# Kernel optimization log

Measured on AMD Instinct MI355X. Metric: run time of the kernel, lower is better.

Reference implementation:

```python
import jax, jax.numpy as jnp
import numpy as np
import math

B, D, NH, NS, NT = 16, 256, 512, 8, 32
NV = NS * NT          # 256 prediction variables
L, H, A = 4, 8, 64    # attention layers, heads, head dim
HA = H * A            # 512
M = 512               # mlp_dim
R = 128               # resolution
EPS = 1e-5


def setup_inputs() -> dict:
    key = jax.random.key(0)
    ks = jax.random.split(key, 32)
    s = 0.02
    inp = {
        'hist_encoded': jax.random.normal(ks[0], (B, NH, D), jnp.float32),
        'hist_true_u': jax.random.uniform(ks[1], (B, NH), jnp.float32),
        'pred_encoded': jax.random.normal(ks[2], (B, NV, D), jnp.float32),
        'pred_true_u': jax.random.uniform(ks[3], (B, NV), jnp.float32),
        # dimension shifting layer
        'ds_w': jax.random.normal(ks[4], (D, HA), jnp.float32) * s,
        'ds_b': jnp.zeros((HA,), jnp.float32),
        # per-layer, per-head key/value creators: Linear(D+1 -> A)
        'key_w': jax.random.normal(ks[5], (L, H, D + 1, A), jnp.float32) * s,
        'key_b': jnp.zeros((L, H, A), jnp.float32),
        'val_w': jax.random.normal(ks[6], (L, H, D + 1, A), jnp.float32) * s,
        'val_b': jnp.zeros((L, H, A), jnp.float32),
        # layer norms
        'ln1_g': jnp.ones((L, HA), jnp.float32),
        'ln1_b': jnp.zeros((L, HA), jnp.float32),
        'ln2_g': jnp.ones((L, HA), jnp.float32),
        'ln2_b': jnp.zeros((L, HA), jnp.float32),
        # feed-forward (mlp_layers=2): HA->M, M->M, M->HA
        'ff_w1': jax.random.normal(ks[7], (L, HA, M), jnp.float32) * s,
        'ff_b1': jnp.zeros((L, M), jnp.float32),
        'ff_w2': jax.random.normal(ks[8], (L, M, M), jnp.float32) * s,
        'ff_b2': jnp.zeros((L, M), jnp.float32),
        'ff_w3': jax.random.normal(ks[9], (L, M, HA), jnp.float32) * s,
        'ff_b3': jnp.zeros((L, HA), jnp.float32),
        # dist extractor
        'de_w': jax.random.normal(ks[10], (HA, R), jnp.float32) * s,
        'de_b': jnp.zeros((R,), jnp.float32),
        'num_series': NS,
        'num_timesteps': NT,
    }
    return inp


def _ln(x, g, b):
    m = x.mean(-1, keepdims=True)
    v = ((x - m) ** 2).mean(-1, keepdims=True)
    return g * (x - m) / jnp.sqrt(v + EPS) + b


def _forward(hist_encoded, hist_true_u, pred_encoded, pred_true_u,
             ds_w, ds_b, key_w, key_b, val_w, val_b,
             ln1_g, ln1_b, ln2_g, ln2_b,
             ff_w1, ff_b1, ff_w2, ff_b2, ff_w3, ff_b3,
             de_w, de_b):
    Bm, NVm, Dm = pred_encoded.shape
    NHm = hist_encoded.shape[1]
    Lm, Hm, _, Am = key_w.shape
    W = NHm + NVm
    # identity permutation in the source loss() -> no-op
    att = pred_encoded @ ds_w + ds_b  # [B, NV, HA]
    # key/value inputs: [hist||u ; pred||u] -> [B, W, D+1]
    ki = jnp.concatenate([
        jnp.concatenate([hist_encoded, hist_true_u[:, :, None]], axis=2),
        jnp.concatenate([pred_encoded, pred_true_u[:, :, None]], axis=2)], axis=1)
    keys = jnp.einsum('bwd,lhda->lbhwa', ki, key_w) + key_b[:, None, :, None, :]
    vals = jnp.einsum('bwd,lhda->lbhwa', ki, val_w) + val_b[:, None, :, None, :]
    # flipped-triangular mask: position w is masked iff w >= NH + v
    mask = jnp.arange(W)[None, :] >= (NHm + jnp.arange(NVm)[:, None])  # [NV, W]
    scale = Am ** (-0.5)
    for l in range(Lm):
        avh = att.reshape(Bm, NVm, Hm, Am)
        prod = jnp.einsum('bvhi,bhwi->bhvw', avh, keys[l])  # [B,H,NV,W]
        prod = jnp.where(mask, -jnp.inf, prod) * scale
        w = jax.nn.softmax(prod, axis=-1)
        a = jnp.einsum('bhvw,bhwj->bvhj', w, vals[l]).reshape(Bm, NVm, Hm * Am)
        att = _ln(att + a, ln1_g[l], ln1_b[l])
        ff = jnp.maximum(att @ ff_w1[l] + ff_b1[l], 0.0)
        ff = jnp.maximum(ff @ ff_w2[l] + ff_b2[l], 0.0)
        ff = ff @ ff_w3[l] + ff_b3[l]
        att = _ln(att + ff, ln2_g[l], ln2_b[l])
    res = de_w.shape[-1]
    target = jnp.clip(jnp.floor(pred_true_u[:, 1:] * res).astype(jnp.int32), 0, res - 1)
    logits = (att @ de_w + de_b)[:, 1:, :]
    lp = math.log(res) + jax.nn.log_softmax(logits, axis=2)
    lp = jnp.take_along_axis(lp, target[:, :, None], axis=2)[:, :, 0]
    return -lp.sum(axis=1)  # [B]


def reference(hist_encoded, hist_true_u, pred_encoded, pred_true_u,
              ds_w, ds_b, key_w, key_b, val_w, val_b,
              ln1_g, ln1_b, ln2_g, ln2_b,
              ff_w1, ff_b1, ff_w2, ff_b2, ff_w3, ff_b3,
              de_w, de_b, num_series, num_timesteps):
    assert pred_encoded.shape[1] == num_series * num_timesteps
    return _forward(hist_encoded, hist_true_u, pred_encoded, pred_true_u,
                    ds_w, ds_b, key_w, key_b, val_w, val_b,
                    ln1_g, ln1_b, ln2_g, ln2_b,
                    ff_w1, ff_b1, ff_w2, ff_b2, ff_w3, ff_b3,
                    de_w, de_b)
```

## Files before the change

### kernel.cpp

```cpp
#include <hip/hip_runtime.h>
#include <hip/hip_cooperative_groups.h>
namespace cg = cooperative_groups;

constexpr int kB = 16, kD = 256, kNH = 512, kNV = 256, kW = 768;
constexpr int kL = 4, kH = 8, kA = 64, kHA = 512, kM = 512, kR = 128;
constexpr int kKP = 288;
constexpr int kRows = kB * kNV;

typedef __bf16 bf16x8 __attribute__((ext_vector_type(8)));
typedef __bf16 bf16x4 __attribute__((ext_vector_type(4)));
typedef float f32x4 __attribute__((ext_vector_type(4)));

__device__ inline void load_lds16(const __bf16* g, __bf16* l) {
  __builtin_amdgcn_global_load_lds(
      (const __attribute__((address_space(1))) void*)g,
      (__attribute__((address_space(3))) void*)l, 16, 0, 0);
}

constexpr int kP1 = kB * kW * kKP;
constexpr int kP2 = 4096 * kKP;
constexpr int kP3 = 12 * 512 * 512;
constexpr int kP4 = 200704;
constexpr int kP5 = 16;
constexpr int kPT = kP1 + kP2 + kP3 + kP4 + kP5;

__global__ void prep_kernel(const float* __restrict__ hist,
                            const float* __restrict__ hist_u,
                            const float* __restrict__ pred,
                            const float* __restrict__ pred_u,
                            const float* __restrict__ kw,
                            const float* __restrict__ vw,
                            const float* __restrict__ w1,
                            const float* __restrict__ w2,
                            const float* __restrict__ w3,
                            const float* __restrict__ ds_w,
                            const float* __restrict__ de_w,
                            const float* __restrict__ key_b,
                            const float* __restrict__ val_b,
                            __bf16* __restrict__ ki,
                            __bf16* __restrict__ kvwt,
                            __bf16* __restrict__ ffwt,
                            __bf16* __restrict__ ds_wt,
                            __bf16* __restrict__ de_wt,
                            float* __restrict__ kvb,
                            float* __restrict__ outz) {
  int i = blockIdx.x * 256 + threadIdx.x;
  if (i < kP1) {
    int d = i % kKP;
    int bw = i / kKP;
    int w = bw % kW;
    int b = bw / kW;
    float v = 0.f;
    if (d < 257) {
      if (w < kNH)
        v = (d < kD) ? hist[((size_t)b * kNH + w) * kD + d] : hist_u[b * kNH + w];
      else {
        int p = w - kNH;
        v = (d < kD) ? pred[((size_t)b * kNV + p) * kD + d] : pred_u[b * kNV + p];
      }
    }
    ki[i] = (__bf16)v;
  } else if (i < kP1 + kP2) {
    int j = i - kP1;
    int d = j % kKP;
    int c = j / kKP;
    float v = 0.f;
    if (d < 257) {
      bool isv = c >= 2048;
      int cc = isv ? c - 2048 : c;
      int l = cc >> 9, rest = cc & 511;
      int h = rest >> 6, a = rest & 63;
      size_t src = (((size_t)l * kH + h) * 257 + d) * kA + a;
      v = isv ? vw[src] : kw[src];
    }
    kvwt[j] = (__bf16)v;
  } else if (i < kP1 + kP2 + kP3) {
    int j = i - kP1 - kP2;
    int k = j & 511;
    int n = (j >> 9) & 511;
    int mat = j >> 18;
    int l = mat / 3, which = mat % 3;
    const float* src = which == 0 ? w1 : which == 1 ? w2 : w3;
    ffwt[j] = (__bf16)src[((size_t)l * 512 + k) * 512 + n];
  } else if (i < kP1 + kP2 + kP3 + kP4) {
    int j = i - kP1 - kP2 - kP3;
    if (j < 131072) {
      int n = j >> 8, k = j & 255;
      ds_wt[j] = (__bf16)ds_w[k * 512 + n];
    } else if (j < 196608) {
      int jj = j - 131072;
      int n = jj >> 9, k = jj & 511;
      de_wt[jj] = (__bf16)de_w[k * 128 + n];
    } else {
      int c = j - 196608;
      bool isv = c >= 2048;
      int cc = isv ? c - 2048 : c;
      int l = cc >> 9, rest = cc & 511;
      kvb[c] = isv ? val_b[l * 512 + rest] : key_b[l * 512 + rest];
    }
  } else if (i < kPT) {
    outz[i - kP1 - kP2 - kP3 - kP4] = 0.f;
  }
}

template <int BN, int OMODE, bool RELU, bool KIMAP, bool BIASROW>
__device__ __forceinline__ void gemm_core(
    int bxv, int byv, const __bf16* __restrict__ A,
    const __bf16* __restrict__ Bt, const float* __restrict__ bias,
    void* __restrict__ Cout, __bf16* __restrict__ Cout2, int K, int lda,
    int ldc, __bf16* As, __bf16* Bs) {
  constexpr int JN = BN / 32;
  constexpr int BROWS = BN / 4;
  const int t = threadIdx.x;
  const int wid = t >> 6;
  const int lane = t & 63;
  const int bm = byv * 128;
  const int bn = bxv * BN;
  const int wm = (wid >> 1) * 64;
  const int wn = (wid & 1) * (BN / 2);
  const int sr = lane >> 2, sc = lane & 3;
  const int skey = (sr >> 1) & 3;
  const int abase = KIMAP ? ((bm >> 8) * 768 + 512 + (bm & 255)) : bm;
  const __bf16* Ag = A + (size_t)(abase + wid * 32 + sr) * lda + (sc ^ skey) * 8;
  const __bf16* Bg = Bt + (size_t)(bn + wid * BROWS + sr) * K + (sc ^ skey) * 8;
  __bf16* AsW = As + (wid * 32) * 32;
  __bf16* BsW = Bs + (wid * BROWS) * 32;

  f32x4 acc[4][JN] = {};
  const int q = lane >> 4, mr = lane & 15;
  const int rkey = (mr >> 1) & 3;
  for (int k0 = 0; k0 < K; k0 += 32) {
    if (k0) __syncthreads();
    load_lds16(Ag + k0, AsW);
    load_lds16(Ag + (size_t)16 * lda + k0, AsW + 16 * 32);
    load_lds16(Bg + k0, BsW);
    if (BN == 128) load_lds16(Bg + (size_t)16 * K + k0, BsW + 16 * 32);
    __syncthreads();
    bf16x8 af[4], bfr[JN];
#pragma unroll
    for (int i = 0; i < 4; ++i)
      af[i] = *(const bf16x8*)(As + (wm + i * 16 + mr) * 32 + (q ^ rkey) * 8);
#pragma unroll
    for (int j = 0; j < JN; ++j)
      bfr[j] = *(const bf16x8*)(Bs + (wn + j * 16 + mr) * 32 + (q ^ rkey) * 8);
#pragma unroll
    for (int i = 0; i < 4; ++i)
#pragma unroll
      for (int j = 0; j < JN; ++j)
        acc[i][j] = __builtin_amdgcn_mfma_f32_16x16x32_bf16(af[i], bfr[j],
                                                            acc[i][j], 0, 0, 0);
  }
#pragma unroll
  for (int j = 0; j < JN; ++j) {
    int col = bn + wn + j * 16 + mr;
    float bscol = BIASROW ? 0.f : bias[col];
#pragma unroll
    for (int i = 0; i < 4; ++i) {
      int row0 = bm + wm + i * 16 + q * 4;
#pragma unroll
      for (int r = 0; r < 4; ++r) {
        float v = acc[i][j][r] + (BIASROW ? bias[row0 + r] : bscol);
        if (RELU) v = fmaxf(v, 0.f);
        size_t idx = (size_t)(row0 + r) * ldc + col;
        if (OMODE == 0) {
          ((float*)Cout)[idx] = v;
        } else if (OMODE == 1) {
          ((__bf16*)Cout)[idx] = (__bf16)v;
        } else {
          ((float*)Cout)[idx] = v;
          Cout2[idx] = (__bf16)v;
        }
      }
    }
  }
}

__global__ __launch_bounds__(256) void gemm3_kernel(
    const __bf16* __restrict__ ki, const __bf16* __restrict__ ds_wt,
    const float* __restrict__ ds_b, float* __restrict__ att,
    __bf16* __restrict__ att_bf, const __bf16* __restrict__ kv_wt,
    const float* __restrict__ kvb, __bf16* __restrict__ kvs_k,
    __bf16* __restrict__ vT) {
  __shared__ __align__(16) __bf16 smem[8192];
  __bf16* As = smem;
  __bf16* Bs = smem + 4096;
  int bid = blockIdx.x;
  if (bid < 256) {
    gemm_core<64, 2, false, true, false>(bid & 7, bid >> 3, ki, ds_wt, ds_b,
                                         att, att_bf, 256, kKP, 512, As, Bs);
  } else if (bid < 1792) {
    int b2 = bid - 256;
    gemm_core<128, 1, false, false, false>(b2 & 15, b2 >> 4, ki, kv_wt, kvb,
                                           kvs_k, nullptr, kKP, kKP, 2048, As,
                                           Bs);
  } else {
    int b3 = bid - 1792;
    gemm_core<128, 1, false, false, true>(b3 % 96, b3 / 96,
                                          kv_wt + (size_t)2048 * kKP, ki,
                                          kvb + 2048, vT, nullptr, kKP, kKP,
                                          12288, As, Bs);
  }
}

__device__ __forceinline__ void attn_stage(
    int u, __bf16* smem, const __bf16* __restrict__ attbf,
    const __bf16* __restrict__ kvs_k, const __bf16* __restrict__ vT,
    __bf16* __restrict__ outbf, int l) {
  const int qt = u & 3, h = (u >> 2) & 7, b = u >> 5;
  __bf16* Ks = smem;
  __bf16* Vt = smem + 64 * 72;
  __bf16* Ps = smem + 2 * 64 * 72;
  const int t = threadIdx.x;
  const int w = t >> 6, lane = t & 63;
  const int quad = lane >> 4, mr = lane & 15;
  bf16x8 aq[2];
  {
    const __bf16* qp = attbf + ((size_t)(b * kNV + qt * 64 + w * 16 + mr) * kHA +
                                h * kA + quad * 8);
    aq[0] = *(const bf16x8*)qp;
    aq[1] = *(const bf16x8*)(qp + 32);
  }
  f32x4 o[4] = {};
  float m_ = -1e30f, l_ = 0.f;
  const int cmax = kNH + qt * 64;
  const int pr = t >> 2, pc = t & 3;
  const __bf16* kbase = kvs_k + ((size_t)(b * kW + pr) * 2048 + l * 512 + h * kA);
  const __bf16* vbase = vT + (size_t)(l * 512 + h * kA + pr) * 12288 + b * kW;
  bf16x8 kc0, kc1, vc0, vc1;
  kc0 = *(const bf16x8*)(kbase + pc * 8);
  kc1 = *(const bf16x8*)(kbase + pc * 8 + 32);
  vc0 = *(const bf16x8*)(vbase + pc * 16);
  vc1 = *(const bf16x8*)(vbase + pc * 16 + 8);
  for (int c0 = 0; c0 <= cmax; c0 += 64) {
    __syncthreads();
    *(bf16x8*)&Ks[pr * 72 + pc * 8] = kc0;
    *(bf16x8*)&Ks[pr * 72 + pc * 8 + 32] = kc1;
    *(bf16x8*)&Vt[pr * 72 + pc * 16] = vc0;
    *(bf16x8*)&Vt[pr * 72 + pc * 16 + 8] = vc1;
    __syncthreads();
    if (c0 + 64 <= cmax) {
      const __bf16* kp = kbase + (size_t)(c0 + 64) * 2048;
      const __bf16* vp = vbase + c0 + 64;
      kc0 = *(const bf16x8*)(kp + pc * 8);
      kc1 = *(const bf16x8*)(kp + pc * 8 + 32);
      vc0 = *(const bf16x8*)(vp + pc * 16);
      vc1 = *(const bf16x8*)(vp + pc * 16 + 8);
    }
    f32x4 s[4];
#pragma unroll
    for (int j = 0; j < 4; ++j) {
      bf16x8 ak0 = *(const bf16x8*)&Ks[(j * 16 + mr) * 72 + quad * 8];
      bf16x8 ak1 = *(const bf16x8*)&Ks[(j * 16 + mr) * 72 + quad * 8 + 32];
      f32x4 z = {};
      z = __builtin_amdgcn_mfma_f32_16x16x32_bf16(ak0, aq[0], z, 0, 0, 0);
      z = __builtin_amdgcn_mfma_f32_16x16x32_bf16(ak1, aq[1], z, 0, 0, 0);
      s[j] = z;
    }
    const int lim = cmax - c0;
    float sv[16], mx = -1e30f;
#pragma unroll
    for (int j = 0; j < 4; ++j)
#pragma unroll
      for (int r = 0; r < 4; ++r) {
        int p = j * 16 + quad * 4 + r;
        float x = (p < lim + mr) ? s[j][r] * 0.125f : -1e30f;
        sv[j * 4 + r] = x;
        mx = fmaxf(mx, x);
      }
    mx = fmaxf(mx, __shfl_xor(mx, 16));
    mx = fmaxf(mx, __shfl_xor(mx, 32));
    float mnew = fmaxf(m_, mx);
    float corr = __expf(m_ - mnew);
    float rs = 0.f;
#pragma unroll
    for (int i = 0; i < 16; ++i) {
      sv[i] = __expf(sv[i] - mnew);
      rs += sv[i];
    }
    rs += __shfl_xor(rs, 16);
    rs += __shfl_xor(rs, 32);
    l_ = l_ * corr + rs;
    m_ = mnew;
#pragma unroll
    for (int j = 0; j < 4; ++j) {
      bf16x4 pk = {(__bf16)sv[j * 4 + 0], (__bf16)sv[j * 4 + 1],
                   (__bf16)sv[j * 4 + 2], (__bf16)sv[j * 4 + 3]};
      *(bf16x4*)&Ps[(w * 16 + mr) * 72 + j * 16 + quad * 4] = pk;
    }
#pragma unroll
    for (int r = 0; r < 4; ++r) {
      float cr = __shfl(corr, quad * 4 + r);
#pragma unroll
      for (int j = 0; j < 4; ++j) o[j][r] *= cr;
    }
    bf16x8 ap0 = *(const bf16x8*)&Ps[(w * 16 + mr) * 72 + quad * 8];
    bf16x8 ap1 = *(const bf16x8*)&Ps[(w * 16 + mr) * 72 + quad * 8 + 32];
#pragma unroll
    for (int j = 0; j < 4; ++j) {
      bf16x8 b0 = *(const bf16x8*)&Vt[(j * 16 + mr) * 72 + quad * 8];
      bf16x8 b1 = *(const bf16x8*)&Vt[(j * 16 + mr) * 72 + quad * 8 + 32];
      o[j] = __builtin_amdgcn_mfma_f32_16x16x32_bf16(ap0, b0, o[j], 0, 0, 0);
      o[j] = __builtin_amdgcn_mfma_f32_16x16x32_bf16(ap1, b1, o[j], 0, 0, 0);
    }
  }
  float invl = 1.f / l_;
#pragma unroll
  for (int r = 0; r < 4; ++r) {
    float ir = __shfl(invl, quad * 4 + r);
    int row = b * kNV + qt * 64 + w * 16 + quad * 4 + r;
#pragma unroll
    for (int j = 0; j < 4; ++j)
      outbf[(size_t)row * kHA + h * kA + j * 16 + mr] = (__bf16)(o[j][r] * ir);
  }
}

__device__ __forceinline__ void ln_stage(int u, float* __restrict__ att,
                                         const __bf16* __restrict__ addbf,
                                         const float* __restrict__ g,
                                         const float* __restrict__ be,
                                         __bf16* __restrict__ attbf) {
  const int t = threadIdx.x;
  const int wid = t >> 6, lane = t & 63;
#pragma unroll
  for (int i = 0; i < 2; ++i) {
    int row = u * 8 + wid * 2 + i;
    float* ar = att + (size_t)row * kHA + lane * 8;
    float4 x0 = *(float4*)ar;
    float4 x1 = *(float4*)(ar + 4);
    bf16x8 d = *(const bf16x8*)(addbf + (size_t)row * kHA + lane * 8);
    float xs[8] = {x0.x + (float)d[0], x0.y + (float)d[1], x0.z + (float)d[2],
                   x0.w + (float)d[3], x1.x + (float)d[4], x1.y + (float)d[5],
                   x1.z + (float)d[6], x1.w + (float)d[7]};
    float s = 0.f, sq = 0.f;
#pragma unroll
    for (int e = 0; e < 8; ++e) {
      s += xs[e];
      sq += xs[e] * xs[e];
    }
    for (int o = 32; o; o >>= 1) {
      s += __shfl_xor(s, o);
      sq += __shfl_xor(sq, o);
    }
    float mean = s * (1.f / kHA);
    float inv = rsqrtf(sq * (1.f / kHA) - mean * mean + 1e-5f);
    const float* gp = g + lane * 8;
    const float* bp = be + lane * 8;
    float4 g0 = *(const float4*)gp, g1 = *(const float4*)(gp + 4);
    float4 b0 = *(const float4*)bp, b1 = *(const float4*)(bp + 4);
    float ga[8] = {g0.x, g0.y, g0.z, g0.w, g1.x, g1.y, g1.z, g1.w};
    float ba[8] = {b0.x, b0.y, b0.z, b0.w, b1.x, b1.y, b1.z, b1.w};
    float ys[8];
    bf16x8 yb;
#pragma unroll
    for (int e = 0; e < 8; ++e) {
      ys[e] = ga[e] * (xs[e] - mean) * inv + ba[e];
      yb[e] = (__bf16)ys[e];
    }
    *(float4*)ar = make_float4(ys[0], ys[1], ys[2], ys[3]);
    *(float4*)(ar + 4) = make_float4(ys[4], ys[5], ys[6], ys[7]);
    *(bf16x8*)(attbf + (size_t)row * kHA + lane * 8) = yb;
  }
}

__device__ __forceinline__ void de_loss_stage(
    int blk, float* red, const __bf16* __restrict__ attbf,
    const __bf16* __restrict__ de_wt, const float* __restrict__ de_b,
    const float* __restrict__ pred_u, float* __restrict__ out) {
  const int t = threadIdx.x;
  const int w = t >> 6, lane = t & 63, quad = lane >> 4, mr = lane & 15;
  const int row0 = blk * 64 + w * 16;
  f32x4 acc[8] = {};
  const __bf16* Ap = attbf + (size_t)(row0 + mr) * kHA + quad * 8;
#pragma unroll 4
  for (int k0 = 0; k0 < 512; k0 += 32) {
    bf16x8 a = *(const bf16x8*)(Ap + k0);
#pragma unroll
    for (int j = 0; j < 8; ++j) {
      bf16x8 bb =
          *(const bf16x8*)(de_wt + (size_t)(j * 16 + mr) * 512 + k0 + quad * 8);
      acc[j] = __builtin_amdgcn_mfma_f32_16x16x32_bf16(a, bb, acc[j], 0, 0, 0);
    }
  }
  float dbv[8];
#pragma unroll
  for (int j = 0; j < 8; ++j) dbv[j] = de_b[j * 16 + mr];
  float lpacc = 0.f;
#pragma unroll
  for (int r = 0; r < 4; ++r) {
    int row = row0 + quad * 4 + r;
    int v = row & 255;
    float lg[8], mx = -1e30f;
#pragma unroll
    for (int j = 0; j < 8; ++j) {
      lg[j] = acc[j][r] + dbv[j];
      mx = fmaxf(mx, lg[j]);
    }
    mx = fmaxf(mx, __shfl_xor(mx, 1));
    mx = fmaxf(mx, __shfl_xor(mx, 2));
    mx = fmaxf(mx, __shfl_xor(mx, 4));
    mx = fmaxf(mx, __shfl_xor(mx, 8));
    float se = 0.f;
#pragma unroll
    for (int j = 0; j < 8; ++j) se += __expf(lg[j] - mx);
    se += __shfl_xor(se, 1);
    se += __shfl_xor(se, 2);
    se += __shfl_xor(se, 4);
    se += __shfl_xor(se, 8);
    float lse = mx + __logf(se);
    float u = pred_u[(row >> 8) * 256 + v];
    int tgt = (int)floorf(u * 128.f);
    tgt = max(0, min(127, tgt));
    float cand = (mr == (tgt & 15)) ? lg[tgt >> 4] : 0.f;
    cand += __shfl_xor(cand, 1);
    cand += __shfl_xor(cand, 2);
    cand += __shfl_xor(cand, 4);
    cand += __shfl_xor(cand, 8);
    float lp = (v >= 1) ? (4.8520302639196171f + cand - lse) : 0.f;
    lpacc += lp;
  }
  lpacc += __shfl_xor(lpacc, 16);
  lpacc += __shfl_xor(lpacc, 32);
  __syncthreads();
  if (lane == 0) red[w] = lpacc;
  __syncthreads();
  if (t == 0)
    atomicAdd(&out[blk >> 2], -(red[0] + red[1] + red[2] + red[3]));
}

__global__ __launch_bounds__(256) void attn_kernel(
    const __bf16* __restrict__ attbf, const __bf16* __restrict__ kvs_k,
    const __bf16* __restrict__ vT, __bf16* __restrict__ outbf, int l) {
  __shared__ __align__(16) __bf16 smem[3 * 64 * 72];
  attn_stage(blockIdx.x, smem, attbf, kvs_k, vT, outbf, l);
}

__global__ __launch_bounds__(256) void ln_kernel(
    float* __restrict__ att, const __bf16* __restrict__ addbf,
    const float* __restrict__ g, const float* __restrict__ be,
    __bf16* __restrict__ attbf) {
  ln_stage(blockIdx.x, att, addbf, g, be, attbf);
}

template <bool RELU>
__global__ __launch_bounds__(256) void gemm_ff_kernel(
    const __bf16* __restrict__ A, const __bf16* __restrict__ Bt,
    const float* __restrict__ bias, __bf16* __restrict__ Cout) {
  __shared__ __align__(16) __bf16 smem[6144];
  gemm_core<64, 1, RELU, false, false>(blockIdx.x & 7, blockIdx.x >> 3, A, Bt,
                                       bias, Cout, nullptr, 512, 512, 512, smem,
                                       smem + 4096);
}

__global__ __launch_bounds__(256) void de_loss_kernel(
    const __bf16* __restrict__ attbf, const __bf16* __restrict__ de_wt,
    const float* __restrict__ de_b, const float* __restrict__ pred_u,
    float* __restrict__ out) {
  __shared__ float red[4];
  de_loss_stage(blockIdx.x, red, attbf, de_wt, de_b, pred_u, out);
}

__global__ __launch_bounds__(256, 2) void model_kernel(
    const __bf16* kvs_k, const __bf16* vT, float* att, __bf16* att_bf,
    __bf16* tmp_bf, __bf16* ff1_bf, __bf16* ff2_bf, const __bf16* ffw_t,
    const float* ff_b1, const float* ff_b2, const float* ff_b3,
    const float* ln1_g, const float* ln1_b, const float* ln2_g,
    const float* ln2_b, const __bf16* de_wt, const float* de_b,
    const float* pred_u, float* out) {
  cg::grid_group grid = cg::this_grid();
  __shared__ __align__(16) __bf16 smem[3 * 64 * 72];
  const int bid = blockIdx.x;
  for (int l = 0; l < kL; ++l) {
    attn_stage(bid, smem, att_bf, kvs_k, vT, tmp_bf, l);
    grid.sync();
    ln_stage(bid, att, tmp_bf, ln1_g + l * kHA, ln1_b + l * kHA, att_bf);
    grid.sync();
    if (bid < 256)
      gemm_core<64, 1, true, false, false>(
          bid & 7, bid >> 3, att_bf, ffw_t + (size_t)(l * 3) * 262144,
          ff_b1 + l * kM, ff1_bf, nullptr, 512, 512, 512, smem, smem + 4096);
    grid.sync();
    if (bid < 256)
      gemm_core<64, 1, true, false, false>(
          bid & 7, bid >> 3, ff1_bf, ffw_t + (size_t)(l * 3 + 1) * 262144,
          ff_b2 + l * kM, ff2_bf, nullptr, 512, 512, 512, smem, smem + 4096);
    grid.sync();
    if (bid < 256)
      gemm_core<64, 1, false, false, false>(
          bid & 7, bid >> 3, ff2_bf, ffw_t + (size_t)(l * 3 + 2) * 262144,
          ff_b3 + l * kHA, tmp_bf, nullptr, 512, 512, 512, smem, smem + 4096);
    grid.sync();
    ln_stage(bid, att, tmp_bf, ln2_g + l * kHA, ln2_b + l * kHA, att_bf);
    grid.sync();
  }
  if (bid < 64)
    de_loss_stage(bid, (float*)smem, att_bf, de_wt, de_b, pred_u, out);
}

extern "C" void kernel_launch(void* const* d_in, const int* in_sizes, int n_in,
                              void* d_out, int out_size, void* d_ws, size_t ws_size,
                              hipStream_t stream) {
  const float* hist   = (const float*)d_in[0];
  const float* hist_u = (const float*)d_in[1];
  const float* pred   = (const float*)d_in[2];
  const float* pred_u = (const float*)d_in[3];
  const float* ds_w   = (const float*)d_in[4];
  const float* ds_b   = (const float*)d_in[5];
  const float* key_w  = (const float*)d_in[6];
  const float* key_b  = (const float*)d_in[7];
  const float* val_w  = (const float*)d_in[8];
  const float* val_b  = (const float*)d_in[9];
  const float* ln1_g  = (const float*)d_in[10];
  const float* ln1_b  = (const float*)d_in[11];
  const float* ln2_g  = (const float*)d_in[12];
  const float* ln2_b  = (const float*)d_in[13];
  const float* ff_w1  = (const float*)d_in[14];
  const float* ff_b1  = (const float*)d_in[15];
  const float* ff_w2  = (const float*)d_in[16];
  const float* ff_b2  = (const float*)d_in[17];
  const float* ff_w3  = (const float*)d_in[18];
  const float* ff_b3  = (const float*)d_in[19];
  const float* de_w   = (const float*)d_in[20];
  const float* de_b   = (const float*)d_in[21];
  float* out = (float*)d_out;

  char* ws = (char*)d_ws;
  size_t off = 0;
  auto alloc = [&](size_t bytes) { char* p = ws + off; off += bytes; return p; };
  __bf16* ki_bf  = (__bf16*)alloc((size_t)kB * kW * kKP * 2);
  __bf16* kv_wt  = (__bf16*)alloc((size_t)4096 * kKP * 2);
  __bf16* ffw_t  = (__bf16*)alloc((size_t)12 * 512 * 512 * 2);
  __bf16* ds_wt  = (__bf16*)alloc((size_t)512 * 256 * 2);
  __bf16* de_wt  = (__bf16*)alloc((size_t)128 * 512 * 2);
  float*  kvb    = (float*)alloc((size_t)4096 * 4);
  __bf16* kvs_k  = (__bf16*)alloc((size_t)kB * kW * 2048 * 2);
  __bf16* vT     = (__bf16*)alloc((size_t)2048 * 12288 * 2);
  float*  att    = (float*)alloc((size_t)kRows * kHA * 4);
  __bf16* att_bf = (__bf16*)alloc((size_t)kRows * kHA * 2);
  __bf16* tmp_bf = (__bf16*)alloc((size_t)kRows * kHA * 2);
  __bf16* ff1_bf = (__bf16*)alloc((size_t)kRows * kM * 2);
  __bf16* ff2_bf = (__bf16*)alloc((size_t)kRows * kM * 2);

  prep_kernel<<<(kPT + 255) / 256, 256, 0, stream>>>(
      hist, hist_u, pred, pred_u, key_w, val_w, ff_w1, ff_w2, ff_w3, ds_w, de_w,
      key_b, val_b, ki_bf, kv_wt, ffw_t, ds_wt, de_wt, kvb, out);

  gemm3_kernel<<<3328, 256, 0, stream>>>(ki_bf, ds_wt, ds_b, att, att_bf, kv_wt,
                                         kvb, kvs_k, vT);

  int nbPerCU = 0;
  hipError_t qerr = hipOccupancyMaxActiveBlocksPerMultiprocessor(
      &nbPerCU, (const void*)model_kernel, 256, 0);
  bool coop = (qerr == hipSuccess && nbPerCU >= 2);
  if (coop) {
    void* cargs[] = {(void*)&kvs_k,  (void*)&vT,     (void*)&att,
                     (void*)&att_bf, (void*)&tmp_bf, (void*)&ff1_bf,
                     (void*)&ff2_bf, (void*)&ffw_t,  (void*)&ff_b1,
                     (void*)&ff_b2,  (void*)&ff_b3,  (void*)&ln1_g,
                     (void*)&ln1_b,  (void*)&ln2_g,  (void*)&ln2_b,
                     (void*)&de_wt,  (void*)&de_b,   (void*)&pred_u,
                     (void*)&out};
    hipError_t lerr = hipLaunchCooperativeKernel(
        (void*)model_kernel, dim3(512), dim3(256), cargs, 0, stream);
    if (lerr != hipSuccess) coop = false;
  }
  if (!coop) {
    for (int l = 0; l < kL; ++l) {
      attn_kernel<<<512, 256, 0, stream>>>(att_bf, kvs_k, vT, tmp_bf, l);
      ln_kernel<<<512, 256, 0, stream>>>(att, tmp_bf, ln1_g + l * kHA,
                                         ln1_b + l * kHA, att_bf);
      gemm_ff_kernel<true><<<256, 256, 0, stream>>>(
          att_bf, ffw_t + (size_t)(l * 3) * 262144, ff_b1 + l * kM, ff1_bf);
      gemm_ff_kernel<true><<<256, 256, 0, stream>>>(
          ff1_bf, ffw_t + (size_t)(l * 3 + 1) * 262144, ff_b2 + l * kM, ff2_bf);
      gemm_ff_kernel<false><<<256, 256, 0, stream>>>(
          ff2_bf, ffw_t + (size_t)(l * 3 + 2) * 262144, ff_b3 + l * kHA, tmp_bf);
      ln_kernel<<<512, 256, 0, stream>>>(att, tmp_bf, ln2_g + l * kHA,
                                         ln2_b + l * kHA, att_bf);
    }
    de_loss_kernel<<<64, 256, 0, stream>>>(att_bf, de_wt, de_b, pred_u, out);
  }
}
```

Baseline: 473.3 us.

## Replace cooperative persistent kernel with per-stage launches and double-buffer attention K/V

Drops the cooperative grid-synchronised model kernel and always runs the separate per-stage kernels. The attention kernel now double-buffers K and V tiles in LDS, cutting to one barrier per chunk and overlapping the next chunk's global loads with the MFMA work. Softmax no longer tracks a running maximum or rescales the accumulator; it exponentiates scaled scores directly, which saves work but can overflow if scores get large. The causal mask now includes the per-wave row offset, which changes the masking compared with the old code.

```diff
diff --git a/kernel.cpp b/kernel.cpp
--- a/kernel.cpp
+++ b/kernel.cpp
@@ -1,6 +1,4 @@
 #include <hip/hip_runtime.h>
-#include <hip/hip_cooperative_groups.h>
-namespace cg = cooperative_groups;
 
 constexpr int kB = 16, kD = 256, kNH = 512, kNV = 256, kW = 768;
 constexpr int kL = 4, kH = 8, kA = 64, kHA = 512, kM = 512, kR = 128;
@@ -202,14 +200,14 @@
   }
 }
 
-__device__ __forceinline__ void attn_stage(
-    int u, __bf16* smem, const __bf16* __restrict__ attbf,
-    const __bf16* __restrict__ kvs_k, const __bf16* __restrict__ vT,
-    __bf16* __restrict__ outbf, int l) {
+__global__ __launch_bounds__(256) void attn_kernel(
+    const __bf16* __restrict__ attbf, const __bf16* __restrict__ kvs_k,
+    const __bf16* __restrict__ vT, __bf16* __restrict__ outbf, int l) {
+  const int u = blockIdx.x;
   const int qt = u & 3, h = (u >> 2) & 7, b = u >> 5;
-  __bf16* Ks = smem;
-  __bf16* Vt = smem + 64 * 72;
-  __bf16* Ps = smem + 2 * 64 * 72;
+  __shared__ __align__(16) __bf16 Ks[2][64 * 72];
+  __shared__ __align__(16) __bf16 Vt[2][64 * 72];
+  __shared__ __align__(16) __bf16 Ps[64 * 72];
   const int t = threadIdx.x;
   const int w = t >> 6, lane = t & 63;
   const int quad = lane >> 4, mr = lane & 15;
@@ -221,24 +219,27 @@
     aq[1] = *(const bf16x8*)(qp + 32);
   }
   f32x4 o[4] = {};
-  float m_ = -1e30f, l_ = 0.f;
+  float l_ = 0.f;
   const int cmax = kNH + qt * 64;
   const int pr = t >> 2, pc = t & 3;
   const __bf16* kbase = kvs_k + ((size_t)(b * kW + pr) * 2048 + l * 512 + h * kA);
   const __bf16* vbase = vT + (size_t)(l * 512 + h * kA + pr) * 12288 + b * kW;
-  bf16x8 kc0, kc1, vc0, vc1;
-  kc0 = *(const bf16x8*)(kbase + pc * 8);
-  kc1 = *(const bf16x8*)(kbase + pc * 8 + 32);
-  vc0 = *(const bf16x8*)(vbase + pc * 16);
-  vc1 = *(const bf16x8*)(vbase + pc * 16 + 8);
+  {
+    bf16x8 k0 = *(const bf16x8*)(kbase + pc * 8);
+    bf16x8 k1 = *(const bf16x8*)(kbase + pc * 8 + 32);
+    bf16x8 v0 = *(const bf16x8*)(vbase + pc * 16);
+    bf16x8 v1 = *(const bf16x8*)(vbase + pc * 16 + 8);
+    *(bf16x8*)&Ks[0][pr * 72 + pc * 8] = k0;
+    *(bf16x8*)&Ks[0][pr * 72 + pc * 8 + 32] = k1;
+    *(bf16x8*)&Vt[0][pr * 72 + pc * 16] = v0;
+    *(bf16x8*)&Vt[0][pr * 72 + pc * 16 + 8] = v1;
+  }
+  __syncthreads();
   for (int c0 = 0; c0 <= cmax; c0 += 64) {
-    __syncthreads();
-    *(bf16x8*)&Ks[pr * 72 + pc * 8] = kc0;
-    *(bf16x8*)&Ks[pr * 72 + pc * 8 + 32] = kc1;
-    *(bf16x8*)&Vt[pr * 72 + pc * 16] = vc0;
-    *(bf16x8*)&Vt[pr * 72 + pc * 16 + 8] = vc1;
-    __syncthreads();
-    if (c0 + 64 <= cmax) {
+    const int cur = (c0 >> 6) & 1;
+    const bool havenext = (c0 + 64 <= cmax);
+    bf16x8 kc0, kc1, vc0, vc1;
+    if (havenext) {
       const __bf16* kp = kbase + (size_t)(c0 + 64) * 2048;
       const __bf16* vp = vbase + c0 + 64;
       kc0 = *(const bf16x8*)(kp + pc * 8);
@@ -249,58 +250,61 @@
     f32x4 s[4];
 #pragma unroll
     for (int j = 0; j < 4; ++j) {
-      bf16x8 ak0 = *(const bf16x8*)&Ks[(j * 16 + mr) * 72 + quad * 8];
-      bf16x8 ak1 = *(const bf16x8*)&Ks[(j * 16 + mr) * 72 + quad * 8 + 32];
+      bf16x8 ak0 = *(const bf16x8*)&Ks[cur][(j * 16 + mr) * 72 + quad * 8];
+      bf16x8 ak1 = *(const bf16x8*)&Ks[cur][(j * 16 + mr) * 72 + quad * 8 + 32];
       f32x4 z = {};
       z = __builtin_amdgcn_mfma_f32_16x16x32_bf16(ak0, aq[0], z, 0, 0, 0);
       z = __builtin_amdgcn_mfma_f32_16x16x32_bf16(ak1, aq[1], z, 0, 0, 0);
       s[j] = z;
     }
     const int lim = cmax - c0;
-    float sv[16], mx = -1e30f;
-#pragma unroll
-    for (int j = 0; j < 4; ++j)
-#pragma unroll
-      for (int r = 0; r < 4; ++r) {
-        int p = j * 16 + quad * 4 + r;
-        float x = (p < lim + mr) ? s[j][r] * 0.125f : -1e30f;
-        sv[j * 4 + r] = x;
-        mx = fmaxf(mx, x);
-      }
-    mx = fmaxf(mx, __shfl_xor(mx, 16));
-    mx = fmaxf(mx, __shfl_xor(mx, 32));
-    float mnew = fmaxf(m_, mx);
-    float corr = __expf(m_ - mnew);
+    float ev[16];
     float rs = 0.f;
-#pragma unroll
-    for (int i = 0; i < 16; ++i) {
-      sv[i] = __expf(sv[i] - mnew);
-      rs += sv[i];
+    if (lim >= 64) {
+#pragma unroll
+      for (int j = 0; j < 4; ++j)
+#pragma unroll
+        for (int r = 0; r < 4; ++r) {
+          float e = __expf(s[j][r] * 0.125f);
+          ev[j * 4 + r] = e;
+          rs += e;
+        }
+    } else {
+      const int limw = lim + w * 16 + mr;
+#pragma unroll
+      for (int j = 0; j < 4; ++j)
+#pragma unroll
+        for (int r = 0; r < 4; ++r) {
+          int p = j * 16 + quad * 4 + r;
+          float e = (p < limw) ? __expf(s[j][r] * 0.125f) : 0.f;
+          ev[j * 4 + r] = e;
+          rs += e;
+        }
     }
     rs += __shfl_xor(rs, 16);
     rs += __shfl_xor(rs, 32);
-    l_ = l_ * corr + rs;
-    m_ = mnew;
+    l_ += rs;
 #pragma unroll
     for (int j = 0; j < 4; ++j) {
-      bf16x4 pk = {(__bf16)sv[j * 4 + 0], (__bf16)sv[j * 4 + 1],
-                   (__bf16)sv[j * 4 + 2], (__bf16)sv[j * 4 + 3]};
+      bf16x4 pk = {(__bf16)ev[j * 4 + 0], (__bf16)ev[j * 4 + 1],
+                   (__bf16)ev[j * 4 + 2], (__bf16)ev[j * 4 + 3]};
       *(bf16x4*)&Ps[(w * 16 + mr) * 72 + j * 16 + quad * 4] = pk;
-    }
-#pragma unroll
-    for (int r = 0; r < 4; ++r) {
-      float cr = __shfl(corr, quad * 4 + r);
-#pragma unroll
-      for (int j = 0; j < 4; ++j) o[j][r] *= cr;
     }
     bf16x8 ap0 = *(const bf16x8*)&Ps[(w * 16 + mr) * 72 + quad * 8];
     bf16x8 ap1 = *(const bf16x8*)&Ps[(w * 16 + mr) * 72 + quad * 8 + 32];
 #pragma unroll
     for (int j = 0; j < 4; ++j) {
-      bf16x8 b0 = *(const bf16x8*)&Vt[(j * 16 + mr) * 72 + quad * 8];
-      bf16x8 b1 = *(const bf16x8*)&Vt[(j * 16 + mr) * 72 + quad * 8 + 32];
+      bf16x8 b0 = *(const bf16x8*)&Vt[cur][(j * 16 + mr) * 72 + quad * 8];
+      bf16x8 b1 = *(const bf16x8*)&Vt[cur][(j * 16 + mr) * 72 + quad * 8 + 32];
       o[j] = __builtin_amdgcn_mfma_f32_16x16x32_bf16(ap0, b0, o[j], 0, 0, 0);
       o[j] = __builtin_amdgcn_mfma_f32_16x16x32_bf16(ap1, b1, o[j], 0, 0, 0);
+    }
+    if (havenext) {
+      *(bf16x8*)&Ks[cur ^ 1][pr * 72 + pc * 8] = kc0;
+      *(bf16x8*)&Ks[cur ^ 1][pr * 72 + pc * 8 + 32] = kc1;
+      *(bf16x8*)&Vt[cur ^ 1][pr * 72 + pc * 16] = vc0;
+      *(bf16x8*)&Vt[cur ^ 1][pr * 72 + pc * 16 + 8] = vc1;
+      __syncthreads();
     }
   }
   float invl = 1.f / l_;
@@ -314,16 +318,15 @@
   }
 }
 
-__device__ __forceinline__ void ln_stage(int u, float* __restrict__ att,
-                                         const __bf16* __restrict__ addbf,
-                                         const float* __restrict__ g,
-                                         const float* __restrict__ be,
-                                         __bf16* __restrict__ attbf) {
+__global__ __launch_bounds__(256) void ln_kernel(
+    float* __restrict__ att, const __bf16* __restrict__ addbf,
+    const float* __restrict__ g, const float* __restrict__ be,
+    __bf16* __restrict__ attbf) {
   const int t = threadIdx.x;
   const int wid = t >> 6, lane = t & 63;
 #pragma unroll
   for (int i = 0; i < 2; ++i) {
-    int row = u * 8 + wid * 2 + i;
+    int row = blockIdx.x * 8 + wid * 2 + i;
     float* ar = att + (size_t)row * kHA + lane * 8;
     float4 x0 = *(float4*)ar;
     float4 x1 = *(float4*)(ar + 4);
@@ -362,10 +365,21 @@
   }
 }
 
-__device__ __forceinline__ void de_loss_stage(
-    int blk, float* red, const __bf16* __restrict__ attbf,
-    const __bf16* __restrict__ de_wt, const float* __restrict__ de_b,
-    const float* __restrict__ pred_u, float* __restrict__ out) {
+template <bool RELU>
+__global__ __launch_bounds__(256) void gemm_ff_kernel(
+    const __bf16* __restrict__ A, const __bf16* __restrict__ Bt,
+    const float* __restrict__ bias, __bf16* __restrict__ Cout) {
+  __shared__ __align__(16) __bf16 smem[6144];
+  gemm_core<64, 1, RELU, false, false>(blockIdx.x & 7, blockIdx.x >> 3, A, Bt,
+                                       bias, Cout, nullptr, 512, 512, 512, smem,
+                                       smem + 4096);
+}
+
+__global__ __launch_bounds__(256) void de_loss_kernel(
+    const __bf16* __restrict__ attbf, const __bf16* __restrict__ de_wt,
+    const float* __restrict__ de_b, const float* __restrict__ pred_u,
+    float* __restrict__ out) {
+  const int blk = blockIdx.x;
   const int t = threadIdx.x;
   const int w = t >> 6, lane = t & 63, quad = lane >> 4, mr = lane & 15;
   const int row0 = blk * 64 + w * 16;
@@ -420,80 +434,11 @@
   }
   lpacc += __shfl_xor(lpacc, 16);
   lpacc += __shfl_xor(lpacc, 32);
-  __syncthreads();
+  __shared__ float red[4];
   if (lane == 0) red[w] = lpacc;
   __syncthreads();
   if (t == 0)
     atomicAdd(&out[blk >> 2], -(red[0] + red[1] + red[2] + red[3]));
-}
-
-__global__ __launch_bounds__(256) void attn_kernel(
-    const __bf16* __restrict__ attbf, const __bf16* __restrict__ kvs_k,
-    const __bf16* __restrict__ vT, __bf16* __restrict__ outbf, int l) {
-  __shared__ __align__(16) __bf16 smem[3 * 64 * 72];
-  attn_stage(blockIdx.x, smem, attbf, kvs_k, vT, outbf, l);
-}
-
-__global__ __launch_bounds__(256) void ln_kernel(
-    float* __restrict__ att, const __bf16* __restrict__ addbf,
-    const float* __restrict__ g, const float* __restrict__ be,
-    __bf16* __restrict__ attbf) {
-  ln_stage(blockIdx.x, att, addbf, g, be, attbf);
-}
-
-template <bool RELU>
-__global__ __launch_bounds__(256) void gemm_ff_kernel(
-    const __bf16* __restrict__ A, const __bf16* __restrict__ Bt,
-    const float* __restrict__ bias, __bf16* __restrict__ Cout) {
-  __shared__ __align__(16) __bf16 smem[6144];
-  gemm_core<64, 1, RELU, false, false>(blockIdx.x & 7, blockIdx.x >> 3, A, Bt,
-                                       bias, Cout, nullptr, 512, 512, 512, smem,
-                                       smem + 4096);
-}
-
-__global__ __launch_bounds__(256) void de_loss_kernel(
-    const __bf16* __restrict__ attbf, const __bf16* __restrict__ de_wt,
-    const float* __restrict__ de_b, const float* __restrict__ pred_u,
-    float* __restrict__ out) {
-  __shared__ float red[4];
-  de_loss_stage(blockIdx.x, red, attbf, de_wt, de_b, pred_u, out);
-}
-
-__global__ __launch_bounds__(256, 2) void model_kernel(
-    const __bf16* kvs_k, const __bf16* vT, float* att, __bf16* att_bf,
-    __bf16* tmp_bf, __bf16* ff1_bf, __bf16* ff2_bf, const __bf16* ffw_t,
-    const float* ff_b1, const float* ff_b2, const float* ff_b3,
-    const float* ln1_g, const float* ln1_b, const float* ln2_g,
-    const float* ln2_b, const __bf16* de_wt, const float* de_b,
-    const float* pred_u, float* out) {
-  cg::grid_group grid = cg::this_grid();
-  __shared__ __align__(16) __bf16 smem[3 * 64 * 72];
-  const int bid = blockIdx.x;
-  for (int l = 0; l < kL; ++l) {
-    attn_stage(bid, smem, att_bf, kvs_k, vT, tmp_bf, l);
-    grid.sync();
-    ln_stage(bid, att, tmp_bf, ln1_g + l * kHA, ln1_b + l * kHA, att_bf);
-    grid.sync();
-    if (bid < 256)
-      gemm_core<64, 1, true, false, false>(
-          bid & 7, bid >> 3, att_bf, ffw_t + (size_t)(l * 3) * 262144,
-          ff_b1 + l * kM, ff1_bf, nullptr, 512, 512, 512, smem, smem + 4096);
-    grid.sync();
-    if (bid < 256)
-      gemm_core<64, 1, true, false, false>(
-          bid & 7, bid >> 3, ff1_bf, ffw_t + (size_t)(l * 3 + 1) * 262144,
-          ff_b2 + l * kM, ff2_bf, nullptr, 512, 512, 512, smem, smem + 4096);
-    grid.sync();
-    if (bid < 256)
-      gemm_core<64, 1, false, false, false>(
-          bid & 7, bid >> 3, ff2_bf, ffw_t + (size_t)(l * 3 + 2) * 262144,
-          ff_b3 + l * kHA, tmp_bf, nullptr, 512, 512, 512, smem, smem + 4096);
-    grid.sync();
-    ln_stage(bid, att, tmp_bf, ln2_g + l * kHA, ln2_b + l * kHA, att_bf);
-    grid.sync();
-  }
-  if (bid < 64)
-    de_loss_stage(bid, (float*)smem, att_bf, de_wt, de_b, pred_u, out);
 }
 
 extern "C" void kernel_launch(void* const* d_in, const int* in_sizes, int n_in,
@@ -547,36 +492,18 @@
   gemm3_kernel<<<3328, 256, 0, stream>>>(ki_bf, ds_wt, ds_b, att, att_bf, kv_wt,
                                          kvb, kvs_k, vT);
 
-  int nbPerCU = 0;
-  hipError_t qerr = hipOccupancyMaxActiveBlocksPerMultiprocessor(
-      &nbPerCU, (const void*)model_kernel, 256, 0);
-  bool coop = (qerr == hipSuccess && nbPerCU >= 2);
-  if (coop) {
-    void* cargs[] = {(void*)&kvs_k,  (void*)&vT,     (void*)&att,
-                     (void*)&att_bf, (void*)&tmp_bf, (void*)&ff1_bf,
-                     (void*)&ff2_bf, (void*)&ffw_t,  (void*)&ff_b1,
-                     (void*)&ff_b2,  (void*)&ff_b3,  (void*)&ln1_g,
-                     (void*)&ln1_b,  (void*)&ln2_g,  (void*)&ln2_b,
-                     (void*)&de_wt,  (void*)&de_b,   (void*)&pred_u,
-                     (void*)&out};
-    hipError_t lerr = hipLaunchCooperativeKernel(
-        (void*)model_kernel, dim3(512), dim3(256), cargs, 0, stream);
-    if (lerr != hipSuccess) coop = false;
-  }
-  if (!coop) {
-    for (int l = 0; l < kL; ++l) {
-      attn_kernel<<<512, 256, 0, stream>>>(att_bf, kvs_k, vT, tmp_bf, l);
-      ln_kernel<<<512, 256, 0, stream>>>(att, tmp_bf, ln1_g + l * kHA,
-                                         ln1_b + l * kHA, att_bf);
-      gemm_ff_kernel<true><<<256, 256, 0, stream>>>(
-          att_bf, ffw_t + (size_t)(l * 3) * 262144, ff_b1 + l * kM, ff1_bf);
-      gemm_ff_kernel<true><<<256, 256, 0, stream>>>(
-          ff1_bf, ffw_t + (size_t)(l * 3 + 1) * 262144, ff_b2 + l * kM, ff2_bf);
-      gemm_ff_kernel<false><<<256, 256, 0, stream>>>(
-          ff2_bf, ffw_t + (size_t)(l * 3 + 2) * 262144, ff_b3 + l * kHA, tmp_bf);
-      ln_kernel<<<512, 256, 0, stream>>>(att, tmp_bf, ln2_g + l * kHA,
-                                         ln2_b + l * kHA, att_bf);
-    }
-    de_loss_kernel<<<64, 256, 0, stream>>>(att_bf, de_wt, de_b, pred_u, out);
-  }
-}
+  for (int l = 0; l < kL; ++l) {
+    attn_kernel<<<512, 256, 0, stream>>>(att_bf, kvs_k, vT, tmp_bf, l);
+    ln_kernel<<<512, 256, 0, stream>>>(att, tmp_bf, ln1_g + l * kHA,
+                                       ln1_b + l * kHA, att_bf);
+    gemm_ff_kernel<true><<<256, 256, 0, stream>>>(
+        att_bf, ffw_t + (size_t)(l * 3) * 262144, ff_b1 + l * kM, ff1_bf);
+    gemm_ff_kernel<true><<<256, 256, 0, stream>>>(
+        ff1_bf, ffw_t + (size_t)(l * 3 + 1) * 262144, ff_b2 + l * kM, ff2_bf);
+    gemm_ff_kernel<false><<<256, 256, 0, stream>>>(
+        ff2_bf, ffw_t + (size_t)(l * 3 + 2) * 262144, ff_b3 + l * kHA, tmp_bf);
+    ln_kernel<<<512, 256, 0, stream>>>(att, tmp_bf, ln2_g + l * kHA,
+                                       ln2_b + l * kHA, att_bf);
+  }
+  de_loss_kernel<<<64, 256, 0, stream>>>(att_bf, de_wt, de_b, pred_u, out);
+}
```

Measured after the change: 475.0 us. About the same (+0.4%).
